# Kernel optimization log

Hardware: AMD Instinct MI355X
Metric: run time of the kernel (lower is better)

Reference implementation:

```python
import jax, jax.numpy as jnp
import numpy as np

N = 500_000
N_ATOMS = 5
T = 8                # angle triplets per (residue, bead) table row
CONT_LEN = 36
GATE_OFFSET = 1
NUM_EXPERTS = 18
BEAD_COL = 36
MAX_BEADS = 4
ANGLE_WEIGHT = 1.0
EPS = 1e-8
MIN_LEN = 0.02


def setup_inputs() -> dict:
    key = jax.random.key(0)
    ks = jax.random.split(key, 8)
    x = jax.random.uniform(ks[0], (N, 38), dtype=jnp.float32)
    # gate column holds residue id in [1, num_experts]; bead column in [0, max_beads)
    res = jax.random.randint(ks[1], (N,), 1, NUM_EXPERTS + 1).astype(jnp.float32)
    bead = jax.random.randint(ks[2], (N,), 0, MAX_BEADS).astype(jnp.float32)
    x = x.at[:, CONT_LEN + 1].set(res)
    x = x.at[:, BEAD_COL].set(bead)
    y_true = jax.random.normal(ks[3], (N, N_ATOMS * 3), dtype=jnp.float32)
    y_pred = jax.random.normal(ks[4], (N, N_ATOMS * 3), dtype=jnp.float32)
    mask = (jax.random.uniform(ks[5], (N, N_ATOMS * 3)) < 0.85).astype(jnp.float32)
    # -1 entries act as invalid-triplet sentinels (trip_ok branch)
    trip = jax.random.randint(ks[6], (NUM_EXPERTS, MAX_BEADS, T, 3), -1, N_ATOMS, dtype=jnp.int32)
    valid = jax.random.randint(ks[7], (NUM_EXPERTS, MAX_BEADS, T), 0, 2, dtype=jnp.int32)
    return {"x": x, "y_true": y_true, "y_pred": y_pred, "mask": mask,
            "angle_triplets_table": trip, "angle_valid_table": valid}


def _atom_mse(true, pred, m):
    # masked per-atom squared error, normalized by count of valid atoms per sample
    se_atom = jnp.sum(jnp.square(true - pred) * m, axis=-1)          # [N, A]
    atom_valid = jnp.any(m > 0.0, axis=-1).astype(se_atom.dtype)     # [N, A]
    num = jnp.sum(se_atom * atom_valid, axis=-1)
    den = jnp.sum(atom_valid, axis=-1) + EPS
    return jnp.mean(num / den)


def _angle_loss(x, true, pred, m, trip_table, valid_table):
    gate = x[:, CONT_LEN + 1]
    gate = jnp.where(jnp.isfinite(gate), gate, 0.0)
    res_id = jnp.clip(jnp.round(gate).astype(jnp.int32) - GATE_OFFSET, 0, NUM_EXPERTS - 1)
    bead = x[:, BEAD_COL]
    bead = jnp.where(jnp.isfinite(bead), bead, 0.0)
    bead_id = jnp.clip(jnp.round(bead).astype(jnp.int32), 0, MAX_BEADS - 1)

    atom_valid = jnp.any(m > 0.0, axis=-1)                           # [N, A]
    trip = trip_table[res_id, bead_id]                               # [N, T, 3]
    base_valid = valid_table[res_id, bead_id]                        # [N, T]
    trip_ok = jnp.all(trip >= 0, axis=-1)
    ts = jnp.maximum(trip, 0)
    i_idx, j_idx, k_idx = ts[..., 0], ts[..., 1], ts[..., 2]         # [N, T]

    rows = jnp.arange(true.shape[0])[:, None]
    vi = atom_valid[rows, i_idx]
    vj = atom_valid[rows, j_idx]
    vk = atom_valid[rows, k_idx]
    ti, tj, tk = true[rows, i_idx], true[rows, j_idx], true[rows, k_idx]   # [N, T, 3]
    pi, pj, pk = pred[rows, i_idx], pred[rows, j_idx], pred[rows, k_idx]

    v1t, v2t, v1p, v2p = ti - tj, tk - tj, pi - pj, pk - pj
    ml2 = jnp.float32(MIN_LEN * MIN_LEN)
    sq = lambda v: jnp.sum(jnp.square(v), axis=-1)
    l1t2, l2t2, l1p2, l2p2 = sq(v1t), sq(v2t), sq(v1p), sq(v2p)

    valid = (trip_ok & (base_valid > 0) & vi & vj & vk
             & (l1t2 > ml2) & (l2t2 > ml2) & (l1p2 > ml2) & (l2p2 > ml2))

    unit = lambda v, l2: v * jax.lax.rsqrt(jnp.maximum(l2, ml2))[..., None]
    u1t, u2t = unit(v1t, l1t2), unit(v2t, l2t2)
    u1p, u2p = unit(v1p, l1p2), unit(v2p, l2p2)

    clip = lambda c: jnp.clip(c, -1.0 + 1e-6, 1.0 - 1e-6)
    cos_t = clip(jnp.sum(u1t * u2t, axis=-1))
    cos_p = clip(jnp.sum(u1p * u2p, axis=-1))
    sin_t = jnp.linalg.norm(jnp.cross(u1t, u2t), axis=-1)
    sin_p = jnp.linalg.norm(jnp.cross(u1p, u2p), axis=-1)

    per_ang = jnp.square(cos_p - cos_t) + jnp.square(sin_p - sin_t)
    per_ang = jnp.where(valid, per_ang, 0.0)
    num = jnp.sum(per_ang, axis=-1)
    den = jnp.sum(valid.astype(jnp.float32), axis=-1) + EPS
    return jnp.mean(num / den)


def reference(x, y_true, y_pred, mask, angle_triplets_table, angle_valid_table):
    true = y_true.reshape(-1, N_ATOMS, 3).astype(jnp.float32)
    pred = y_pred.reshape(-1, N_ATOMS, 3).astype(jnp.float32)
    m = mask.reshape(-1, N_ATOMS, 3).astype(jnp.float32)
    atom = _atom_mse(true, pred, m)
    ang = _angle_loss(x, true, pred, m, angle_triplets_table, angle_valid_table)
    return atom + ANGLE_WEIGHT * ang
```

## Files before the change

### kernel.cpp

```cpp
#include <hip/hip_runtime.h>
#include <math.h>

#define NATOMS 5
#define NEXP 18
#define NBEAD 4
#define EPSV 1e-8f
#define ML2 (0.02f * 0.02f)

__global__ void pack_tables(const int* __restrict__ trip, const int* __restrict__ valid,
                            int4* __restrict__ ptbl) {
    int c = blockIdx.x * blockDim.x + threadIdx.x;
    if (c < NEXP * NBEAD) {
        unsigned w[4] = {0u, 0u, 0u, 0u};
#pragma unroll
        for (int t = 0; t < 8; t++) {
            int b = c * 8 + t;
            int i = trip[b * 3 + 0], j = trip[b * 3 + 1], k = trip[b * 3 + 2];
            unsigned ok = (i >= 0 && j >= 0 && k >= 0 && valid[b] > 0) ? 1u : 0u;
            unsigned oi = 3u * (unsigned)min(max(i, 0), NATOMS - 1);
            unsigned oj = 3u * (unsigned)min(max(j, 0), NATOMS - 1);
            unsigned ov = 3u * (unsigned)min(max(k, 0), NATOMS - 1);
            unsigned e = oi | (oj << 4) | (ov << 8) | (ok << 12);
            w[t >> 1] |= e << ((t & 1) * 16);
        }
        ptbl[c] = make_int4((int)w[0], (int)w[1], (int)w[2], (int)w[3]);
    }
}

__global__ __launch_bounds__(256, 5) void loss_kernel(
    const float* __restrict__ xin, const float* __restrict__ y_true,
    const float* __restrict__ y_pred, const float* __restrict__ mask,
    const int4* __restrict__ ptbl, float* __restrict__ partial, int n) {
    __shared__ float scr[8192];

    const int tid = threadIdx.x;
    const int row = blockIdx.x * 256 + tid;
    float* st = scr + (tid << 5);

    float result = 0.0f;
    if (row < n) {
        const size_t rb = (size_t)row * 15;
        const float* gT = y_true + rb;
        const float* gP = y_pred + rb;
        const float* gM = mask + rb;

        float T[15], P[15], M[15];
#pragma unroll
        for (int c = 0; c < 15; c++) T[c] = gT[c];
#pragma unroll
        for (int c = 0; c < 15; c++) P[c] = gP[c];
#pragma unroll
        for (int c = 0; c < 15; c++) M[c] = gM[c];

        float2 gb = *(const float2*)(xin + (size_t)row * 38 + 36);
        float beadf = isfinite(gb.x) ? gb.x : 0.f;
        float gatef = isfinite(gb.y) ? gb.y : 0.f;
        gatef = fminf(fmaxf(gatef, -1e6f), 1e6f);
        beadf = fminf(fmaxf(beadf, -1e6f), 1e6f);
        int res_id = min(max((int)rintf(gatef) - 1, 0), NEXP - 1);
        int bead_id = min(max((int)rintf(beadf), 0), NBEAD - 1);
        int4 pk = ptbl[res_id * NBEAD + bead_id];
        unsigned tw0 = (unsigned)pk.x, tw1 = (unsigned)pk.y;
        unsigned tw2 = (unsigned)pk.z, tw3 = (unsigned)pk.w;

#pragma unroll
        for (int c = 0; c < 15; c++) st[c] = T[c];
#pragma unroll
        for (int c = 0; c < 15; c++) st[16 + c] = P[c];

        float num_a = 0.f, den_a = 0.f;
        unsigned avm2 = 0u;
#pragma unroll
        for (int a = 0; a < 5; a++) {
            bool m0 = M[3 * a + 0] > 0.f;
            bool m1 = M[3 * a + 1] > 0.f;
            bool m2 = M[3 * a + 2] > 0.f;
            float d0 = T[3 * a + 0] - P[3 * a + 0];
            float d1 = T[3 * a + 1] - P[3 * a + 1];
            float d2 = T[3 * a + 2] - P[3 * a + 2];
            float se = (m0 ? d0 * d0 : 0.f) + (m1 ? d1 * d1 : 0.f) + (m2 ? d2 * d2 : 0.f);
            if (m0 || m1 || m2) { num_a += se; den_a += 1.f; avm2 |= 1u << (3 * a); }
        }
        result = num_a / (den_a + EPSV);

        float num_g = 0.f, den_g = 0.f;
#pragma unroll
        for (int t = 0; t < 8; t++) {
            unsigned wrd = (t < 2) ? tw0 : (t < 4) ? tw1 : (t < 6) ? tw2 : tw3;
            unsigned e = (wrd >> ((t & 1) * 16)) & 0xffffu;
            int oi = e & 15, oj = (e >> 4) & 15, ov = (e >> 8) & 15;
            bool wok = ((e >> 12) & 1u) != 0u;

            float tix = st[oi], tiy = st[oi + 1], tiz = st[oi + 2];
            float tjx = st[oj], tjy = st[oj + 1], tjz = st[oj + 2];
            float tkx = st[ov], tky = st[ov + 1], tkz = st[ov + 2];
            float pix = st[16 + oi], piy = st[17 + oi], piz = st[18 + oi];
            float pjx = st[16 + oj], pjy = st[17 + oj], pjz = st[18 + oj];
            float pkx = st[16 + ov], pky = st[17 + ov], pkz = st[18 + ov];

            float v1tx = tix - tjx, v1ty = tiy - tjy, v1tz = tiz - tjz;
            float v2tx = tkx - tjx, v2ty = tky - tjy, v2tz = tkz - tjz;
            float v1px = pix - pjx, v1py = piy - pjy, v1pz = piz - pjz;
            float v2px = pkx - pjx, v2py = pky - pjy, v2pz = pkz - pjz;

            float l1t = fmaf(v1tx, v1tx, fmaf(v1ty, v1ty, v1tz * v1tz));
            float l2t = fmaf(v2tx, v2tx, fmaf(v2ty, v2ty, v2tz * v2tz));
            float l1p = fmaf(v1px, v1px, fmaf(v1py, v1py, v1pz * v1pz));
            float l2p = fmaf(v2px, v2px, fmaf(v2py, v2py, v2pz * v2pz));

            bool okv = wok && ((avm2 >> oi) & 1) && ((avm2 >> oj) & 1) &&
                       ((avm2 >> ov) & 1) && (l1t > ML2) && (l2t > ML2) &&
                       (l1p > ML2) && (l2p > ML2);

            float rt = __builtin_amdgcn_rsqf(fmaxf(l1t, ML2) * fmaxf(l2t, ML2));
            float rp = __builtin_amdgcn_rsqf(fmaxf(l1p, ML2) * fmaxf(l2p, ML2));

            float dott = fmaf(v1tx, v2tx, fmaf(v1ty, v2ty, v1tz * v2tz));
            float dotp = fmaf(v1px, v2px, fmaf(v1py, v2py, v1pz * v2pz));
            float cut = dott * rt;
            float cup = dotp * rp;
            float cost = fminf(fmaxf(cut, -1.f + 1e-6f), 1.f - 1e-6f);
            float cosp = fminf(fmaxf(cup, -1.f + 1e-6f), 1.f - 1e-6f);
            float sint = __builtin_amdgcn_sqrtf(fmaxf(fmaf(-cut, cut, 1.f), 0.f));
            float sinp = __builtin_amdgcn_sqrtf(fmaxf(fmaf(-cup, cup, 1.f), 0.f));

            float dc = cosp - cost, dsn = sinp - sint;
            if (okv) { num_g += fmaf(dc, dc, dsn * dsn); den_g += 1.f; }
        }
        result += num_g / (den_g + EPSV);
    }

#pragma unroll
    for (int off = 32; off > 0; off >>= 1)
        result += __shfl_down(result, off, 64);
    __syncthreads();
    float* red = scr;
    int lane = tid & 63, wv = tid >> 6;
    if (lane == 0) red[wv] = result;
    __syncthreads();
    if (tid == 0) partial[blockIdx.x] = red[0] + red[1] + red[2] + red[3];
}

__global__ __launch_bounds__(256) void reduce_kernel(const float* __restrict__ partial,
                                                     float* __restrict__ out, int nblocks,
                                                     float inv_n) {
    __shared__ float red[4];
    float s = 0.f;
    for (int i = threadIdx.x; i < nblocks; i += 256) s += partial[i];
#pragma unroll
    for (int off = 32; off > 0; off >>= 1) s += __shfl_down(s, off, 64);
    int lane = threadIdx.x & 63, wv = threadIdx.x >> 6;
    if (lane == 0) red[wv] = s;
    __syncthreads();
    if (threadIdx.x == 0) out[0] = (red[0] + red[1] + red[2] + red[3]) * inv_n;
}

extern "C" void kernel_launch(void* const* d_in, const int* in_sizes, int n_in,
                              void* d_out, int out_size, void* d_ws, size_t ws_size,
                              hipStream_t stream) {
    const float* x = (const float*)d_in[0];
    const float* y_true = (const float*)d_in[1];
    const float* y_pred = (const float*)d_in[2];
    const float* mask = (const float*)d_in[3];
    const int* trip = (const int*)d_in[4];
    const int* valid = (const int*)d_in[5];
    float* out = (float*)d_out;

    int4* ptbl = (int4*)d_ws;
    float* partial = (float*)((char*)d_ws + 4096);

    const int n = in_sizes[1] / 15;
    const int blocks = (n + 255) / 256;

    pack_tables<<<1, 128, 0, stream>>>(trip, valid, ptbl);
    loss_kernel<<<blocks, 256, 0, stream>>>(x, y_true, y_pred, mask, ptbl, partial, n);
    reduce_kernel<<<1, 256, 0, stream>>>(partial, out, blocks, 1.0f / (float)n);
}
```

Baseline: 194.3 us.

## Process two rows per thread with loads issued up front and padded LDS stride

Each thread now handles two rows, issuing all global loads for both rows before any compute so more memory traffic is in flight per thread. Mask values are packed into a bitmask early to free registers, the per-thread scratch stride is padded to 33 to avoid LDS bank conflicts, and launch bounds change from 5 to 4 waves per SIMD. The trade-off is higher register pressure and half as many blocks, which may lower occupancy or leave the tail of the grid underused.

```diff
diff --git a/kernel.cpp b/kernel.cpp
--- a/kernel.cpp
+++ b/kernel.cpp
@@ -27,108 +27,144 @@
     }
 }
 
-__global__ __launch_bounds__(256, 5) void loss_kernel(
+__device__ __forceinline__ float row_loss(const float* __restrict__ T,
+                                          const float* __restrict__ P,
+                                          unsigned mbits, int4 pk, float* __restrict__ st) {
+    float num_a = 0.f, den_a = 0.f;
+    unsigned avm2 = 0u;
+#pragma unroll
+    for (int a = 0; a < 5; a++) {
+        unsigned mb = (mbits >> (3 * a)) & 7u;
+        float d0 = T[3 * a + 0] - P[3 * a + 0];
+        float d1 = T[3 * a + 1] - P[3 * a + 1];
+        float d2 = T[3 * a + 2] - P[3 * a + 2];
+        float se = (mb & 1u ? d0 * d0 : 0.f) + (mb & 2u ? d1 * d1 : 0.f) +
+                   (mb & 4u ? d2 * d2 : 0.f);
+        if (mb) { num_a += se; den_a += 1.f; avm2 |= 1u << (3 * a); }
+    }
+    float res = num_a / (den_a + EPSV);
+
+#pragma unroll
+    for (int c = 0; c < 15; c++) st[c] = T[c];
+#pragma unroll
+    for (int c = 0; c < 15; c++) st[16 + c] = P[c];
+
+    unsigned tw0 = (unsigned)pk.x, tw1 = (unsigned)pk.y;
+    unsigned tw2 = (unsigned)pk.z, tw3 = (unsigned)pk.w;
+
+    float num_g = 0.f, den_g = 0.f;
+#pragma unroll
+    for (int t = 0; t < 8; t++) {
+        unsigned wrd = (t < 2) ? tw0 : (t < 4) ? tw1 : (t < 6) ? tw2 : tw3;
+        unsigned e = (wrd >> ((t & 1) * 16)) & 0xffffu;
+        int oi = e & 15, oj = (e >> 4) & 15, ov = (e >> 8) & 15;
+        bool wok = ((e >> 12) & 1u) != 0u;
+
+        float tix = st[oi], tiy = st[oi + 1], tiz = st[oi + 2];
+        float tjx = st[oj], tjy = st[oj + 1], tjz = st[oj + 2];
+        float tkx = st[ov], tky = st[ov + 1], tkz = st[ov + 2];
+        float pix = st[16 + oi], piy = st[17 + oi], piz = st[18 + oi];
+        float pjx = st[16 + oj], pjy = st[17 + oj], pjz = st[18 + oj];
+        float pkx = st[16 + ov], pky = st[17 + ov], pkz = st[18 + ov];
+
+        float v1tx = tix - tjx, v1ty = tiy - tjy, v1tz = tiz - tjz;
+        float v2tx = tkx - tjx, v2ty = tky - tjy, v2tz = tkz - tjz;
+        float v1px = pix - pjx, v1py = piy - pjy, v1pz = piz - pjz;
+        float v2px = pkx - pjx, v2py = pky - pjy, v2pz = pkz - pjz;
+
+        float l1t = fmaf(v1tx, v1tx, fmaf(v1ty, v1ty, v1tz * v1tz));
+        float l2t = fmaf(v2tx, v2tx, fmaf(v2ty, v2ty, v2tz * v2tz));
+        float l1p = fmaf(v1px, v1px, fmaf(v1py, v1py, v1pz * v1pz));
+        float l2p = fmaf(v2px, v2px, fmaf(v2py, v2py, v2pz * v2pz));
+
+        bool okv = wok && ((avm2 >> oi) & 1) && ((avm2 >> oj) & 1) &&
+                   ((avm2 >> ov) & 1) && (l1t > ML2) && (l2t > ML2) &&
+                   (l1p > ML2) && (l2p > ML2);
+
+        float rt = __builtin_amdgcn_rsqf(fmaxf(l1t, ML2) * fmaxf(l2t, ML2));
+        float rp = __builtin_amdgcn_rsqf(fmaxf(l1p, ML2) * fmaxf(l2p, ML2));
+
+        float dott = fmaf(v1tx, v2tx, fmaf(v1ty, v2ty, v1tz * v2tz));
+        float dotp = fmaf(v1px, v2px, fmaf(v1py, v2py, v1pz * v2pz));
+        float cut = dott * rt;
+        float cup = dotp * rp;
+        float cost = fminf(fmaxf(cut, -1.f + 1e-6f), 1.f - 1e-6f);
+        float cosp = fminf(fmaxf(cup, -1.f + 1e-6f), 1.f - 1e-6f);
+        float sint = __builtin_amdgcn_sqrtf(fmaxf(fmaf(-cut, cut, 1.f), 0.f));
+        float sinp = __builtin_amdgcn_sqrtf(fmaxf(fmaf(-cup, cup, 1.f), 0.f));
+
+        float dc = cosp - cost, dsn = sinp - sint;
+        if (okv) { num_g += fmaf(dc, dc, dsn * dsn); den_g += 1.f; }
+    }
+    return res + num_g / (den_g + EPSV);
+}
+
+__global__ __launch_bounds__(256, 4) void loss_kernel(
     const float* __restrict__ xin, const float* __restrict__ y_true,
     const float* __restrict__ y_pred, const float* __restrict__ mask,
     const int4* __restrict__ ptbl, float* __restrict__ partial, int n) {
-    __shared__ float scr[8192];
+    __shared__ float scr[256 * 33];
 
     const int tid = threadIdx.x;
-    const int row = blockIdx.x * 256 + tid;
-    float* st = scr + (tid << 5);
-
-    float result = 0.0f;
-    if (row < n) {
-        const size_t rb = (size_t)row * 15;
-        const float* gT = y_true + rb;
-        const float* gP = y_pred + rb;
-        const float* gM = mask + rb;
-
-        float T[15], P[15], M[15];
-#pragma unroll
-        for (int c = 0; c < 15; c++) T[c] = gT[c];
-#pragma unroll
-        for (int c = 0; c < 15; c++) P[c] = gP[c];
-#pragma unroll
-        for (int c = 0; c < 15; c++) M[c] = gM[c];
-
-        float2 gb = *(const float2*)(xin + (size_t)row * 38 + 36);
-        float beadf = isfinite(gb.x) ? gb.x : 0.f;
-        float gatef = isfinite(gb.y) ? gb.y : 0.f;
+    const int row0 = blockIdx.x * 512 + tid;
+    const int row1 = row0 + 256;
+    const bool v0 = row0 < n, v1 = row1 < n;
+    float* st = scr + tid * 33;
+
+    float T0[15], P0[15], T1[15], P1[15];
+    unsigned mb0 = 0u, mb1 = 0u;
+    float2 gb0 = make_float2(0.f, 0.f), gb1 = make_float2(0.f, 0.f);
+
+    if (v0) {
+        const size_t rb = (size_t)row0 * 15;
+#pragma unroll
+        for (int c = 0; c < 15; c++) T0[c] = y_true[rb + c];
+#pragma unroll
+        for (int c = 0; c < 15; c++) P0[c] = y_pred[rb + c];
+        gb0 = *(const float2*)(xin + (size_t)row0 * 38 + 36);
+        float M0[15];
+#pragma unroll
+        for (int c = 0; c < 15; c++) M0[c] = mask[rb + c];
+#pragma unroll
+        for (int c = 0; c < 15; c++) mb0 |= (M0[c] > 0.f ? 1u : 0u) << c;
+    }
+    if (v1) {
+        const size_t rb = (size_t)row1 * 15;
+#pragma unroll
+        for (int c = 0; c < 15; c++) T1[c] = y_true[rb + c];
+#pragma unroll
+        for (int c = 0; c < 15; c++) P1[c] = y_pred[rb + c];
+        gb1 = *(const float2*)(xin + (size_t)row1 * 38 + 36);
+        float M1[15];
+#pragma unroll
+        for (int c = 0; c < 15; c++) M1[c] = mask[rb + c];
+#pragma unroll
+        for (int c = 0; c < 15; c++) mb1 |= (M1[c] > 0.f ? 1u : 0u) << c;
+    }
+
+    int4 pk0 = make_int4(0, 0, 0, 0), pk1 = make_int4(0, 0, 0, 0);
+    if (v0) {
+        float beadf = isfinite(gb0.x) ? gb0.x : 0.f;
+        float gatef = isfinite(gb0.y) ? gb0.y : 0.f;
         gatef = fminf(fmaxf(gatef, -1e6f), 1e6f);
         beadf = fminf(fmaxf(beadf, -1e6f), 1e6f);
-        int res_id = min(max((int)rintf(gatef) - 1, 0), NEXP - 1);
-        int bead_id = min(max((int)rintf(beadf), 0), NBEAD - 1);
-        int4 pk = ptbl[res_id * NBEAD + bead_id];
-        unsigned tw0 = (unsigned)pk.x, tw1 = (unsigned)pk.y;
-        unsigned tw2 = (unsigned)pk.z, tw3 = (unsigned)pk.w;
-
-#pragma unroll
-        for (int c = 0; c < 15; c++) st[c] = T[c];
-#pragma unroll
-        for (int c = 0; c < 15; c++) st[16 + c] = P[c];
-
-        float num_a = 0.f, den_a = 0.f;
-        unsigned avm2 = 0u;
-#pragma unroll
-        for (int a = 0; a < 5; a++) {
-            bool m0 = M[3 * a + 0] > 0.f;
-            bool m1 = M[3 * a + 1] > 0.f;
-            bool m2 = M[3 * a + 2] > 0.f;
-            float d0 = T[3 * a + 0] - P[3 * a + 0];
-            float d1 = T[3 * a + 1] - P[3 * a + 1];
-            float d2 = T[3 * a + 2] - P[3 * a + 2];
-            float se = (m0 ? d0 * d0 : 0.f) + (m1 ? d1 * d1 : 0.f) + (m2 ? d2 * d2 : 0.f);
-            if (m0 || m1 || m2) { num_a += se; den_a += 1.f; avm2 |= 1u << (3 * a); }
-        }
-        result = num_a / (den_a + EPSV);
-
-        float num_g = 0.f, den_g = 0.f;
-#pragma unroll
-        for (int t = 0; t < 8; t++) {
-            unsigned wrd = (t < 2) ? tw0 : (t < 4) ? tw1 : (t < 6) ? tw2 : tw3;
-            unsigned e = (wrd >> ((t & 1) * 16)) & 0xffffu;
-            int oi = e & 15, oj = (e >> 4) & 15, ov = (e >> 8) & 15;
-            bool wok = ((e >> 12) & 1u) != 0u;
-
-            float tix = st[oi], tiy = st[oi + 1], tiz = st[oi + 2];
-            float tjx = st[oj], tjy = st[oj + 1], tjz = st[oj + 2];
-            float tkx = st[ov], tky = st[ov + 1], tkz = st[ov + 2];
-            float pix = st[16 + oi], piy = st[17 + oi], piz = st[18 + oi];
-            float pjx = st[16 + oj], pjy = st[17 + oj], pjz = st[18 + oj];
-            float pkx = st[16 + ov], pky = st[17 + ov], pkz = st[18 + ov];
-
-            float v1tx = tix - tjx, v1ty = tiy - tjy, v1tz = tiz - tjz;
-            float v2tx = tkx - tjx, v2ty = tky - tjy, v2tz = tkz - tjz;
-            float v1px = pix - pjx, v1py = piy - pjy, v1pz = piz - pjz;
-            float v2px = pkx - pjx, v2py = pky - pjy, v2pz = pkz - pjz;
-
-            float l1t = fmaf(v1tx, v1tx, fmaf(v1ty, v1ty, v1tz * v1tz));
-            float l2t = fmaf(v2tx, v2tx, fmaf(v2ty, v2ty, v2tz * v2tz));
-            float l1p = fmaf(v1px, v1px, fmaf(v1py, v1py, v1pz * v1pz));
-            float l2p = fmaf(v2px, v2px, fmaf(v2py, v2py, v2pz * v2pz));
-
-            bool okv = wok && ((avm2 >> oi) & 1) && ((avm2 >> oj) & 1) &&
-                       ((avm2 >> ov) & 1) && (l1t > ML2) && (l2t > ML2) &&
-                       (l1p > ML2) && (l2p > ML2);
-
-            float rt = __builtin_amdgcn_rsqf(fmaxf(l1t, ML2) * fmaxf(l2t, ML2));
-            float rp = __builtin_amdgcn_rsqf(fmaxf(l1p, ML2) * fmaxf(l2p, ML2));
-
-            float dott = fmaf(v1tx, v2tx, fmaf(v1ty, v2ty, v1tz * v2tz));
-            float dotp = fmaf(v1px, v2px, fmaf(v1py, v2py, v1pz * v2pz));
-            float cut = dott * rt;
-            float cup = dotp * rp;
-            float cost = fminf(fmaxf(cut, -1.f + 1e-6f), 1.f - 1e-6f);
-            float cosp = fminf(fmaxf(cup, -1.f + 1e-6f), 1.f - 1e-6f);
-            float sint = __builtin_amdgcn_sqrtf(fmaxf(fmaf(-cut, cut, 1.f), 0.f));
-            float sinp = __builtin_amdgcn_sqrtf(fmaxf(fmaf(-cup, cup, 1.f), 0.f));
-
-            float dc = cosp - cost, dsn = sinp - sint;
-            if (okv) { num_g += fmaf(dc, dc, dsn * dsn); den_g += 1.f; }
-        }
-        result += num_g / (den_g + EPSV);
-    }
+        int rid = min(max((int)rintf(gatef) - 1, 0), NEXP - 1);
+        int bid = min(max((int)rintf(beadf), 0), NBEAD - 1);
+        pk0 = ptbl[rid * NBEAD + bid];
+    }
+    if (v1) {
+        float beadf = isfinite(gb1.x) ? gb1.x : 0.f;
+        float gatef = isfinite(gb1.y) ? gb1.y : 0.f;
+        gatef = fminf(fmaxf(gatef, -1e6f), 1e6f);
+        beadf = fminf(fmaxf(beadf, -1e6f), 1e6f);
+        int rid = min(max((int)rintf(gatef) - 1, 0), NEXP - 1);
+        int bid = min(max((int)rintf(beadf), 0), NBEAD - 1);
+        pk1 = ptbl[rid * NBEAD + bid];
+    }
+
+    float result = 0.f;
+    if (v0) result += row_loss(T0, P0, mb0, pk0, st);
+    if (v1) result += row_loss(T1, P1, mb1, pk1, st);
 
 #pragma unroll
     for (int off = 32; off > 0; off >>= 1)
@@ -170,7 +206,7 @@
     float* partial = (float*)((char*)d_ws + 4096);
 
     const int n = in_sizes[1] / 15;
-    const int blocks = (n + 255) / 256;
+    const int blocks = (n + 511) / 512;
 
     pack_tables<<<1, 128, 0, stream>>>(trip, valid, ptbl);
     loss_kernel<<<blocks, 256, 0, stream>>>(x, y_true, y_pred, mask, ptbl, partial, n);
```

Result: no change. 194.5 us (+0.1%).

## Stage row data through LDS with coalesced float4 nontemporal loads in 64-thread blocks

Applied to the files above, without the earlier changes.

Each 64-row block now cooperatively loads its y_true, y_pred and mask slices as contiguous float4 nontemporal loads into shared memory, replacing the per-thread strided 15-float scalar loads. Threads then read their own rows from LDS. Blocks shrink to one wavefront, which drops the cross-wave shared reduction and its syncs. This is meant to cut uncoalesced global traffic. It adds a block barrier, and the stride-15 LDS reads may cause bank conflicts, and there are four times as many partial sums to reduce.

```diff
diff --git a/kernel.cpp b/kernel.cpp
--- a/kernel.cpp
+++ b/kernel.cpp
@@ -6,6 +6,9 @@
 #define NBEAD 4
 #define EPSV 1e-8f
 #define ML2 (0.02f * 0.02f)
+
+typedef float vf4a __attribute__((ext_vector_type(4), aligned(16)));
+typedef float vf2u __attribute__((ext_vector_type(2), aligned(4)));
 
 __global__ void pack_tables(const int* __restrict__ trip, const int* __restrict__ valid,
                             int4* __restrict__ ptbl) {
@@ -27,61 +30,83 @@
     }
 }
 
-__global__ __launch_bounds__(256, 5) void loss_kernel(
+__global__ __launch_bounds__(64) void loss_kernel(
     const float* __restrict__ xin, const float* __restrict__ y_true,
     const float* __restrict__ y_pred, const float* __restrict__ mask,
     const int4* __restrict__ ptbl, float* __restrict__ partial, int n) {
-    __shared__ float scr[8192];
+    __shared__ float sT[960];
+    __shared__ float sP[960];
+    __shared__ float sM[960];
 
     const int tid = threadIdx.x;
-    const int row = blockIdx.x * 256 + tid;
-    float* st = scr + (tid << 5);
+    const int rbase = blockIdx.x * 64;
+    const int row = rbase + tid;
+    const size_t dbase = (size_t)rbase * 15;
+    const long long total = (long long)n * 15;
 
-    float result = 0.0f;
+    vf2u gb;
+    gb.x = 0.f; gb.y = 0.f;
+    if (row < n) gb = __builtin_nontemporal_load((const vf2u*)(xin + (size_t)row * 38 + 36));
+
+    const vf4a* qT = (const vf4a*)(y_true + dbase);
+    const vf4a* qP = (const vf4a*)(y_pred + dbase);
+    const vf4a* qM = (const vf4a*)(mask + dbase);
+    vf4a tC[4], pC[4], mC[4];
+    bool ok[4];
+#pragma unroll
+    for (int k = 0; k < 4; k++) {
+        int q = k * 64 + tid;
+        ok[k] = (q < 240) && (dbase + 4 * (long long)q + 4 <= total);
+        if (ok[k]) {
+            tC[k] = __builtin_nontemporal_load(qT + q);
+            pC[k] = __builtin_nontemporal_load(qP + q);
+            mC[k] = __builtin_nontemporal_load(qM + q);
+        }
+    }
+#pragma unroll
+    for (int k = 0; k < 4; k++) {
+        int q = k * 64 + tid;
+        if (ok[k]) {
+            ((vf4a*)sT)[q] = tC[k];
+            ((vf4a*)sP)[q] = pC[k];
+            ((vf4a*)sM)[q] = mC[k];
+        }
+    }
+    __syncthreads();
+
+    float result = 0.f;
     if (row < n) {
-        const size_t rb = (size_t)row * 15;
-        const float* gT = y_true + rb;
-        const float* gP = y_pred + rb;
-        const float* gM = mask + rb;
+        const float* st = sT + tid * 15;
+        const float* sp = sP + tid * 15;
+        const float* sm = sM + tid * 15;
 
-        float T[15], P[15], M[15];
+        unsigned mrow = 0u;
 #pragma unroll
-        for (int c = 0; c < 15; c++) T[c] = gT[c];
-#pragma unroll
-        for (int c = 0; c < 15; c++) P[c] = gP[c];
-#pragma unroll
-        for (int c = 0; c < 15; c++) M[c] = gM[c];
-
-        float2 gb = *(const float2*)(xin + (size_t)row * 38 + 36);
-        float beadf = isfinite(gb.x) ? gb.x : 0.f;
-        float gatef = isfinite(gb.y) ? gb.y : 0.f;
-        gatef = fminf(fmaxf(gatef, -1e6f), 1e6f);
-        beadf = fminf(fmaxf(beadf, -1e6f), 1e6f);
-        int res_id = min(max((int)rintf(gatef) - 1, 0), NEXP - 1);
-        int bead_id = min(max((int)rintf(beadf), 0), NBEAD - 1);
-        int4 pk = ptbl[res_id * NBEAD + bead_id];
-        unsigned tw0 = (unsigned)pk.x, tw1 = (unsigned)pk.y;
-        unsigned tw2 = (unsigned)pk.z, tw3 = (unsigned)pk.w;
-
-#pragma unroll
-        for (int c = 0; c < 15; c++) st[c] = T[c];
-#pragma unroll
-        for (int c = 0; c < 15; c++) st[16 + c] = P[c];
+        for (int c = 0; c < 15; c++) mrow |= (sm[c] > 0.f ? 1u : 0u) << c;
 
         float num_a = 0.f, den_a = 0.f;
         unsigned avm2 = 0u;
 #pragma unroll
         for (int a = 0; a < 5; a++) {
-            bool m0 = M[3 * a + 0] > 0.f;
-            bool m1 = M[3 * a + 1] > 0.f;
-            bool m2 = M[3 * a + 2] > 0.f;
-            float d0 = T[3 * a + 0] - P[3 * a + 0];
-            float d1 = T[3 * a + 1] - P[3 * a + 1];
-            float d2 = T[3 * a + 2] - P[3 * a + 2];
-            float se = (m0 ? d0 * d0 : 0.f) + (m1 ? d1 * d1 : 0.f) + (m2 ? d2 * d2 : 0.f);
-            if (m0 || m1 || m2) { num_a += se; den_a += 1.f; avm2 |= 1u << (3 * a); }
+            unsigned mb = (mrow >> (3 * a)) & 7u;
+            float d0 = st[3 * a + 0] - sp[3 * a + 0];
+            float d1 = st[3 * a + 1] - sp[3 * a + 1];
+            float d2 = st[3 * a + 2] - sp[3 * a + 2];
+            float se = (mb & 1u ? d0 * d0 : 0.f) + (mb & 2u ? d1 * d1 : 0.f) +
+                       (mb & 4u ? d2 * d2 : 0.f);
+            if (mb) { num_a += se; den_a += 1.f; avm2 |= 1u << (3 * a); }
         }
         result = num_a / (den_a + EPSV);
+
+        float beadf = isfinite(gb.x) ? gb.x : 0.f;
+        float gatef = isfinite(gb.y) ? gb.y : 0.f;
+        gatef = fminf(fmaxf(gatef, -1e6f), 1e6f);
+        beadf = fminf(fmaxf(beadf, -1e6f), 1e6f);
+        int rid = min(max((int)rintf(gatef) - 1, 0), NEXP - 1);
+        int bid = min(max((int)rintf(beadf), 0), NBEAD - 1);
+        int4 pk = ptbl[rid * NBEAD + bid];
+        unsigned tw0 = (unsigned)pk.x, tw1 = (unsigned)pk.y;
+        unsigned tw2 = (unsigned)pk.z, tw3 = (unsigned)pk.w;
 
         float num_g = 0.f, den_g = 0.f;
 #pragma unroll
@@ -94,9 +119,9 @@
             float tix = st[oi], tiy = st[oi + 1], tiz = st[oi + 2];
             float tjx = st[oj], tjy = st[oj + 1], tjz = st[oj + 2];
             float tkx = st[ov], tky = st[ov + 1], tkz = st[ov + 2];
-            float pix = st[16 + oi], piy = st[17 + oi], piz = st[18 + oi];
-            float pjx = st[16 + oj], pjy = st[17 + oj], pjz = st[18 + oj];
-            float pkx = st[16 + ov], pky = st[17 + ov], pkz = st[18 + ov];
+            float pix = sp[oi], piy = sp[oi + 1], piz = sp[oi + 2];
+            float pjx = sp[oj], pjy = sp[oj + 1], pjz = sp[oj + 2];
+            float pkx = sp[ov], pky = sp[ov + 1], pkz = sp[ov + 2];
 
             float v1tx = tix - tjx, v1ty = tiy - tjy, v1tz = tiz - tjz;
             float v2tx = tkx - tjx, v2ty = tky - tjy, v2tz = tkz - tjz;
@@ -133,12 +158,7 @@
 #pragma unroll
     for (int off = 32; off > 0; off >>= 1)
         result += __shfl_down(result, off, 64);
-    __syncthreads();
-    float* red = scr;
-    int lane = tid & 63, wv = tid >> 6;
-    if (lane == 0) red[wv] = result;
-    __syncthreads();
-    if (tid == 0) partial[blockIdx.x] = red[0] + red[1] + red[2] + red[3];
+    if (tid == 0) partial[blockIdx.x] = result;
 }
 
 __global__ __launch_bounds__(256) void reduce_kernel(const float* __restrict__ partial,
@@ -170,9 +190,9 @@
     float* partial = (float*)((char*)d_ws + 4096);
 
     const int n = in_sizes[1] / 15;
-    const int blocks = (n + 255) / 256;
+    const int blocks = (n + 63) / 64;
 
     pack_tables<<<1, 128, 0, stream>>>(trip, valid, ptbl);
-    loss_kernel<<<blocks, 256, 0, stream>>>(x, y_true, y_pred, mask, ptbl, partial, n);
+    loss_kernel<<<blocks, 64, 0, stream>>>(x, y_true, y_pred, mask, ptbl, partial, n);
     reduce_kernel<<<1, 256, 0, stream>>>(partial, out, blocks, 1.0f / (float)n);
 }
```

After: 187.0 us. 3.8% less time.
